# Kernel optimization log

Hardware: AMD Instinct MI355X
Metric: run time of the kernel (lower is better)

## Reference

```python
import jax, jax.numpy as jnp
import numpy as np

N = 100000      # nodes
E = 1600000     # edges (before self-loops)
D_IN = 128      # node_attr_size
H = 4           # gat_heads
C = 32          # hidden_size (per-head out channels)
F = H * C       # feature_size = 128
K = 16          # num_clusters
L = 2           # num_gat_layers
EPS = 1e-5
NEG_SLOPE = 0.2  # PyG GATv2Conv default leaky_relu slope


def setup_inputs() -> dict:
    key = jax.random.key(0)
    ks = jax.random.split(key, 8)
    x = jax.random.normal(ks[0], (N, D_IN), jnp.float32)
    edge_index = jax.random.randint(ks[1], (2, E), 0, N, jnp.int32)
    sF = 1.0 / np.sqrt(F).astype(np.float32)
    Wp = jax.random.normal(ks[2], (D_IN, F), jnp.float32) * (1.0 / np.sqrt(D_IN).astype(np.float32))
    bp = jnp.zeros((F,), jnp.float32)
    ln_g = jnp.ones((L, F), jnp.float32)
    ln_b = jnp.zeros((L, F), jnp.float32)
    Wl = jax.random.normal(ks[3], (L, F, H * C), jnp.float32) * sF
    bl = jnp.zeros((L, H * C), jnp.float32)
    Wr = jax.random.normal(ks[4], (L, F, H * C), jnp.float32) * sF
    br = jnp.zeros((L, H * C), jnp.float32)
    att = jax.random.normal(ks[5], (L, H, C), jnp.float32) * (1.0 / np.sqrt(C).astype(np.float32))
    gb = jnp.zeros((L, F), jnp.float32)  # GATv2Conv output bias
    Wc = jax.random.normal(ks[6], (F, K), jnp.float32) * sF
    bc = jnp.zeros((K,), jnp.float32)
    return dict(x=x, edge_index=edge_index, Wp=Wp, bp=bp, ln_g=ln_g, ln_b=ln_b,
                Wl=Wl, bl=bl, Wr=Wr, br=br, att=att, gb=gb, Wc=Wc, bc=bc)


def _layernorm(x, g, b):
    mu = jnp.mean(x, axis=-1, keepdims=True)
    var = jnp.var(x, axis=-1, keepdims=True)
    return (x - mu) * jax.lax.rsqrt(var + EPS) * g + b


def reference(x, edge_index, Wp, bp, ln_g, ln_b, Wl, bl, Wr, br, att, gb, Wc, bc):
    # GATv2Conv adds self-loops by default
    loops = jnp.arange(N, dtype=edge_index.dtype)
    src = jnp.concatenate([edge_index[0], loops])  # message source j
    dst = jnp.concatenate([edge_index[1], loops])  # message target i

    h = x @ Wp + bp  # node_feat_proj -> [N, F]
    for i in range(L):
        identity = h
        hn = _layernorm(h, ln_g[i], ln_b[i])
        x_l = (hn @ Wl[i] + bl[i]).reshape(N, H, C)  # source transform
        x_r = (hn @ Wr[i] + br[i]).reshape(N, H, C)  # target transform
        m = x_l[src] + x_r[dst]                       # [E+N, H, C]
        s = jnp.where(m > 0, m, NEG_SLOPE * m)        # leaky_relu(0.2)
        logits = jnp.einsum('ehc,hc->eh', s, att[i])  # [E+N, H]
        # segment softmax over incoming edges of each target node
        mx = jax.ops.segment_max(logits, dst, num_segments=N)
        a = jnp.exp(logits - mx[dst])
        den = jax.ops.segment_sum(a, dst, num_segments=N)
        alpha = a / den[dst]
        out = jax.ops.segment_sum(x_l[src] * alpha[:, :, None], dst, num_segments=N)
        out = out.reshape(N, F) + gb[i]
        # relu activation, dropout identity (eval), residual add
        h = jax.nn.relu(out) + identity

    classification_output = h @ Wc + bc
    return (classification_output, h)
```

## Files before the change

### kernel.cpp

```cpp
#include <hip/hip_runtime.h>
#include <hip/hip_bf16.h>
#include <math.h>
#include <stdint.h>

#define N_NODES 100000
#define N_EDGES 1600000
#define ET (N_EDGES + N_NODES)
#define FDIM 128
#define NK 16
#define EPS 1e-5f
#define SLOPE 0.2f

typedef __attribute__((ext_vector_type(8))) short bf16x8;
typedef __attribute__((ext_vector_type(4))) float f32x4;
typedef __attribute__((ext_vector_type(2))) _Float16 h2;

__device__ inline unsigned pk_bf16(float a, float b) {
    float2 f; f.x = a; f.y = b;
    __hip_bfloat162 t = __float22bfloat162_rn(f);
    return *reinterpret_cast<unsigned*>(&t);
}
__device__ inline h2 as_h2(unsigned u) { return __builtin_bit_cast(h2, u); }
__device__ inline unsigned as_u(h2 v) { return __builtin_bit_cast(unsigned, v); }

#define SWZ(X, P) __int_as_float(__builtin_amdgcn_ds_swizzle(__float_as_int(X), (P)))
#define DPPF(X, CTRL) __int_as_float(__builtin_amdgcn_mov_dpp(__float_as_int(X), (CTRL), 0xF, 0xF, true))
#define DX1(X) DPPF(X, 0xB1)
#define DX2(X) DPPF(X, 0x4E)
#define DR4(X) DPPF(X, 0x124)
#define DR8(X) DPPF(X, 0x128)
#define DB0(X) DPPF(X, 0x00)
#define DB1(X) DPPF(X, 0x55)
#define DB2(X) DPPF(X, 0xAA)
#define DB3(X) DPPF(X, 0xFF)

__device__ inline float exp2_hw(float x) {
    float r;
    asm("v_exp_f32 %0, %1" : "=v"(r) : "v"(x));
    return r;
}

#define FMAMIX_LO(ACC, U, W) \
    asm("v_fma_mix_f32 %0, %1, %2, %0 op_sel_hi:[1,0,0]" : "+v"(ACC) : "v"(U), "v"(W))
#define FMAMIX_HI(ACC, U, W) \
    asm("v_fma_mix_f32 %0, %1, %2, %0 op_sel:[1,0,0] op_sel_hi:[1,0,0]" : "+v"(ACC) : "v"(U), "v"(W))

__device__ inline int rflm(int v) { return __builtin_amdgcn_readfirstlane(v) & 131071; }


#define NBKT 196
#define BSH 9
#define BSTRIDE 10240
#define P1_EPT 8
#define P1_EPB (256 * P1_EPT)

__global__ __launch_bounds__(256) void part_kernel(const int* __restrict__ ei,
                                                   int* __restrict__ gcount,
                                                   int* __restrict__ staging) {
    __shared__ int hist[NBKT];
    __shared__ int lofs[NBKT];
    __shared__ int gbase[NBKT];
    __shared__ int s[256];
    __shared__ int spk[P1_EPB];
    __shared__ short sbk[P1_EPB];
    int t = threadIdx.x;
    if (t < NBKT) hist[t] = 0;
    __syncthreads();
    int e0 = blockIdx.x * P1_EPB + t;
    int pk[P1_EPT], bk[P1_EPT], rk[P1_EPT];
#pragma unroll
    for (int k = 0; k < P1_EPT; k++) {
        int e = e0 + k * 256;
        bk[k] = -1;
        if (e < ET) {
            int src, dst;
            if (e < N_EDGES) { src = ei[e]; dst = ei[N_EDGES + e]; }
            else             { src = dst = e - N_EDGES; }
            int b = dst >> BSH;
            pk[k] = (src << BSH) | (dst & 511);
            bk[k] = b;
            rk[k] = atomicAdd(&hist[b], 1);
        }
    }
    __syncthreads();
    int v = (t < NBKT) ? hist[t] : 0;
    s[t] = v;
    __syncthreads();
    for (int o = 1; o < 256; o <<= 1) {
        int add = (t >= o) ? s[t - o] : 0;
        __syncthreads();
        s[t] += add;
        __syncthreads();
    }
    if (t < NBKT) {
        lofs[t] = s[t] - v;
        gbase[t] = (v > 0) ? atomicAdd(&gcount[t], v) : 0;
    }
    __syncthreads();
#pragma unroll
    for (int k = 0; k < P1_EPT; k++) {
        if (bk[k] >= 0) {
            int idx = lofs[bk[k]] + rk[k];
            spk[idx] = pk[k];
            sbk[idx] = (short)bk[k];
        }
    }
    __syncthreads();
    int tot = lofs[NBKT - 1] + hist[NBKT - 1];
    for (int i = t; i < tot; i += 256) {
        int b = sbk[i];
        staging[b * BSTRIDE + gbase[b] + (i - lofs[b])] = spk[i];
    }
}

__global__ __launch_bounds__(1024) void bucket_csr_kernel(
        const int* __restrict__ staging, const int* __restrict__ gcount,
        int* __restrict__ off, int* __restrict__ perm) {
    __shared__ int hist[512];
    __shared__ int scn[512];
    __shared__ int cur[512];
    __shared__ int gpre[256];
    int b = blockIdx.x;
    int t = threadIdx.x;
    if (t < 512) hist[t] = 0;
    if (t < 256) gpre[t] = (t < NBKT) ? gcount[t] : 0;
    __syncthreads();
    int sz = gcount[b];
    for (int k = t; k < sz; k += 1024)
        atomicAdd(&hist[staging[b * BSTRIDE + k] & 511], 1);
    __syncthreads();
    int v = (t < 512) ? hist[t] : 0;
    if (t < 512) scn[t] = v;
    __syncthreads();
    for (int o = 1; o < 512; o <<= 1) {
        int add = 0, gadd = 0;
        int tg = t - 512;
        if (t < 512 && t >= o) add = scn[t - o];
        if (tg >= o && tg < 256 && o < 256) gadd = gpre[tg - o];
        __syncthreads();
        if (t < 512) scn[t] += add;
        if (tg >= o && tg < 256 && o < 256) gpre[tg] += gadd;
        __syncthreads();
    }
    int base = gpre[b] - sz;
    if (t < 512) {
        int excl = scn[t] - v;
        int n = (b << BSH) + t;
        if (n < N_NODES) off[n] = base + excl;
        cur[t] = excl;
    }
    if (b == 0 && t == 0) off[N_NODES] = ET;
    __syncthreads();
    for (int k = t; k < sz; k += 1024) {
        int p = staging[b * BSTRIDE + k];
        int slot = atomicAdd(&cur[p & 511], 1);
        perm[base + slot] = p >> BSH;
    }
}


__global__ void swizzle_kernel(const float* __restrict__ Wp,
                               const float* __restrict__ Wl,
                               const float* __restrict__ Wr,
                               ushort* __restrict__ wbp,
                               ushort* __restrict__ wbl0,
                               ushort* __restrict__ wbl1) {
    int bb = blockIdx.x, t = threadIdx.x;
    const float *W0, *W1; ushort* out; int nt;
    if (bb < 8)       { W0 = Wp; W1 = Wp; out = wbp; nt = bb; }
    else if (bb < 24) { W0 = Wl; W1 = Wr; out = wbl0; nt = bb - 8; }
    else              { W0 = Wl + FDIM * FDIM; W1 = Wr + FDIM * FDIM; out = wbl1; nt = bb - 24; }
    int kk = t >> 6, lane = t & 63;
    int n = nt * 16 + (lane & 15);
    int k0 = kk * 32 + (lane >> 4) * 8;
    const float* W = (n < 128) ? (W0 + n) : (W1 + (n - 128));
    float f[8];
#pragma unroll
    for (int j = 0; j < 8; j++) f[j] = W[(size_t)(k0 + j) * FDIM];
    uint4 u;
    u.x = pk_bf16(f[0], f[1]); u.y = pk_bf16(f[2], f[3]);
    u.z = pk_bf16(f[4], f[5]); u.w = pk_bf16(f[6], f[7]);
    *(uint4*)&out[(size_t)((nt * 4 + kk) * 64 + lane) * 8] = u;
}


__global__ __launch_bounds__(256) void ln_gemm2_kernel(
        const float* __restrict__ h,
        const float* __restrict__ g, const float* __restrict__ b,
        const ushort* __restrict__ wb, const float* __restrict__ bl,
        const float* __restrict__ br,
        ushort* __restrict__ xlh, ushort* __restrict__ xrh) {
    __shared__ uint4 fragbuf[4 * 272];
    int wid = (blockIdx.x * 256 + threadIdx.x) >> 6;
    int lane = threadIdx.x & 63;
    if (wid >= N_NODES / 16) return;
    uint4* fb = fragbuf + (threadIdx.x >> 6) * 272;
    int q = lane >> 4, m = lane & 15;
    int row0 = wid * 16;
    const float* hrow = h + (size_t)(row0 + m) * FDIM + q * 32;
    float v[32];
#pragma unroll
    for (int i = 0; i < 8; i++) {
        float4 t4 = *(const float4*)&hrow[i * 4];
        v[i * 4 + 0] = t4.x; v[i * 4 + 1] = t4.y; v[i * 4 + 2] = t4.z; v[i * 4 + 3] = t4.w;
    }
    float s = 0.f, ss = 0.f;
#pragma unroll
    for (int i = 0; i < 32; i++) { s += v[i]; ss += v[i] * v[i]; }
    s  += __shfl_xor(s, 16);  s  += __shfl_xor(s, 32);
    ss += __shfl_xor(ss, 16); ss += __shfl_xor(ss, 32);
    float mu = s * (1.f / 128.f);
    float var = ss * (1.f / 128.f) - mu * mu;
    float rv = rsqrtf(var + EPS);
#pragma unroll
    for (int i = 0; i < 8; i++) {
        float4 gv = *(const float4*)&g[q * 32 + i * 4];
        float4 bv = *(const float4*)&b[q * 32 + i * 4];
        v[i * 4 + 0] = (v[i * 4 + 0] - mu) * rv * gv.x + bv.x;
        v[i * 4 + 1] = (v[i * 4 + 1] - mu) * rv * gv.y + bv.y;
        v[i * 4 + 2] = (v[i * 4 + 2] - mu) * rv * gv.z + bv.z;
        v[i * 4 + 3] = (v[i * 4 + 3] - mu) * rv * gv.w + bv.w;
    }
#pragma unroll
    for (int p = 0; p < 4; p++) {
        uint4 u;
        u.x = pk_bf16(v[p * 8 + 0], v[p * 8 + 1]);
        u.y = pk_bf16(v[p * 8 + 2], v[p * 8 + 3]);
        u.z = pk_bf16(v[p * 8 + 4], v[p * 8 + 5]);
        u.w = pk_bf16(v[p * 8 + 6], v[p * 8 + 7]);
        fb[q * 68 + p * 17 + m] = u;
    }
    bf16x8 A[4];
#pragma unroll
    for (int kk = 0; kk < 4; kk++)
        A[kk] = *(const bf16x8*)&fb[kk * 68 + q * 17 + m];
    const bf16x8* wbv = (const bf16x8*)wb;
    f32x4 acc[16];
    f32x4 z = {0.f, 0.f, 0.f, 0.f};
#pragma unroll
    for (int nt = 0; nt < 16; nt++) acc[nt] = z;
#pragma unroll
    for (int nt = 0; nt < 16; nt++) {
#pragma unroll
        for (int kk = 0; kk < 4; kk++) {
            bf16x8 B = wbv[(nt * 4 + kk) * 64 + lane];
            acc[nt] = __builtin_amdgcn_mfma_f32_16x16x32_bf16(A[kk], B, acc[nt], 0, 0, 0);
        }
    }
#pragma unroll
    for (int nt = 0; nt < 16; nt++) {
        int col = nt * 16 + m;
        if (nt < 8) {
            float bias = bl[col];
#pragma unroll
            for (int r = 0; r < 4; r++) {
                _Float16 hf = (_Float16)(acc[nt][r] + bias);
                xlh[(size_t)(row0 + q * 4 + r) * FDIM + col] = __builtin_bit_cast(ushort, hf);
            }
        } else {
            int c2 = col - 128;
            float bias = br[c2];
#pragma unroll
            for (int r = 0; r < 4; r++) {
                _Float16 hf = (_Float16)(acc[nt][r] + bias);
                xrh[(size_t)(row0 + q * 4 + r) * FDIM + c2] = __builtin_bit_cast(ushort, hf);
            }
        }
    }
}

__global__ __launch_bounds__(256) void proj_kernel(
        const float* __restrict__ x, const ushort* __restrict__ wb,
        const float* __restrict__ bp, float* __restrict__ h) {
    __shared__ uint4 fragbuf[4 * 272];
    int wid = (blockIdx.x * 256 + threadIdx.x) >> 6;
    int lane = threadIdx.x & 63;
    if (wid >= N_NODES / 16) return;
    uint4* fb = fragbuf + (threadIdx.x >> 6) * 272;
    int q = lane >> 4, m = lane & 15;
    int row0 = wid * 16;
    const float* xrow = x + (size_t)(row0 + m) * FDIM + q * 32;
#pragma unroll
    for (int p = 0; p < 4; p++) {
        float4 a = *(const float4*)&xrow[p * 8];
        float4 c = *(const float4*)&xrow[p * 8 + 4];
        uint4 u;
        u.x = pk_bf16(a.x, a.y); u.y = pk_bf16(a.z, a.w);
        u.z = pk_bf16(c.x, c.y); u.w = pk_bf16(c.z, c.w);
        fb[q * 68 + p * 17 + m] = u;
    }
    bf16x8 A[4];
#pragma unroll
    for (int kk = 0; kk < 4; kk++)
        A[kk] = *(const bf16x8*)&fb[kk * 68 + q * 17 + m];
    const bf16x8* wbv = (const bf16x8*)wb;
    f32x4 acc[8];
    f32x4 z = {0.f, 0.f, 0.f, 0.f};
#pragma unroll
    for (int nt = 0; nt < 8; nt++) acc[nt] = z;
#pragma unroll
    for (int nt = 0; nt < 8; nt++) {
#pragma unroll
        for (int kk = 0; kk < 4; kk++) {
            bf16x8 B = wbv[(nt * 4 + kk) * 64 + lane];
            acc[nt] = __builtin_amdgcn_mfma_f32_16x16x32_bf16(A[kk], B, acc[nt], 0, 0, 0);
        }
    }
#pragma unroll
    for (int nt = 0; nt < 8; nt++) {
        int col = nt * 16 + m;
        float bias = bp[col];
#pragma unroll
        for (int r = 0; r < 4; r++)
            h[(size_t)(row0 + q * 4 + r) * FDIM + col] = acc[nt][r] + bias;
    }
}

__global__ __launch_bounds__(256) void final_kernel(const float* __restrict__ h,
                                                    const float* __restrict__ Wc,
                                                    const float* __restrict__ bc,
                                                    float* __restrict__ out) {
    __shared__ float sh[16][128];
    int row0 = blockIdx.x * 16;
    int t = threadIdx.x;
    for (int i = t; i < 512; i += 256) {
        int r = i >> 5, c4 = (i & 31) * 4;
        *(float4*)&sh[r][c4] = *(const float4*)&h[(size_t)(row0 + r) * FDIM + c4];
    }
    __syncthreads();
    int m = t >> 4, k = t & 15;
    float acc = 0.f;
    for (int c = 0; c < 128; c += 4) {
        const float4 xv = *(const float4*)&sh[m][c];
        acc += xv.x * Wc[(c + 0) * NK + k] + xv.y * Wc[(c + 1) * NK + k]
             + xv.z * Wc[(c + 2) * NK + k] + xv.w * Wc[(c + 3) * NK + k];
    }
    out[(size_t)(row0 + m) * NK + k] = acc + bc[k];
}


__global__ __launch_bounds__(256) void gat_agg_kernel(
        const unsigned* __restrict__ xlp, const unsigned* __restrict__ xrp,
        const int* __restrict__ off, const int* __restrict__ perm,
        const float* __restrict__ att, const float* __restrict__ gb,
        float* __restrict__ h) {
    int wave = (blockIdx.x * 256 + threadIdx.x) >> 6;
    unsigned lane = threadIdx.x & 63;
    if (wave >= N_NODES) return;
    int i = wave;
    h2 xrv = as_h2(xrp[(unsigned)i * 64u + lane]);
    const float2 hid = *(const float2*)&h[(size_t)i * FDIM + lane * 2];
    const float2 gbv = *(const float2*)&gb[lane * 2];
    float2 attf = *(const float2*)&att[lane * 2];
    h2 attp; attp[0] = (_Float16)(attf.x * 1.44269504f);
    attp[1] = (_Float16)(attf.y * 1.44269504f);
    const h2 c06 = {(_Float16)0.6f, (_Float16)0.6f};
    const h2 c04 = {(_Float16)0.4f, (_Float16)0.4f};
    bool b0 = lane & 1, b1 = lane & 2;
    int beg = __builtin_amdgcn_readfirstlane(off[i]);
    int end = __builtin_amdgcn_readfirstlane(off[i + 1]);
    float accx = 0.f, accy = 0.f, dloc = 0.f;
    const char* xlB = (const char*)xlp;
    unsigned laneB = lane << 2;

#define GLD(J) (*(const unsigned*)(xlB + ((unsigned)(J) * 256u + laneB)))

#define EDGE_PARTIAL(U, T)                                          \
    {                                                               \
        h2 mm = as_h2(U) + xrv;                                     \
        h2 am = as_h2(as_u(mm) & 0x7FFF7FFFu);                      \
        h2 sv = am * c04 + mm * c06;                                \
        T = __builtin_amdgcn_fdot2(sv, attp, 0.f, false);           \
    }

#define COMPUTE4(U0, U1, U2, U3)                                    \
    {                                                               \
        float t0, t1, t2, t3;                                       \
        EDGE_PARTIAL(U0, t0);                                       \
        EDGE_PARTIAL(U1, t1);                                       \
        EDGE_PARTIAL(U2, t2);                                       \
        EDGE_PARTIAL(U3, t3);                                       \
        float u   = b0 ? t1 : t0;                                   \
        float uu2 = b0 ? t0 : t1;                                   \
        u += DX1(uu2);                                              \
        float vv  = b0 ? t3 : t2;                                   \
        float vv2 = b0 ? t2 : t3;                                   \
        vv += DX1(vv2);                                             \
        float ww  = b1 ? vv : u;                                    \
        float ww2 = b1 ? u : vv;                                    \
        ww += DX2(ww2);                                             \
        ww += DR4(ww);                                              \
        ww += DR8(ww);                                              \
        float ew = exp2_hw(ww);                                     \
        dloc += ew;                                                 \
        float w0 = DB0(ew);                                         \
        float w1 = DB1(ew);                                         \
        float w2 = DB2(ew);                                         \
        float w3 = DB3(ew);                                         \
        FMAMIX_LO(accx, U0, w0); FMAMIX_HI(accy, U0, w0);           \
        FMAMIX_LO(accx, U1, w1); FMAMIX_HI(accy, U1, w1);           \
        FMAMIX_LO(accx, U2, w2); FMAMIX_HI(accy, U2, w2);           \
        FMAMIX_LO(accx, U3, w3); FMAMIX_HI(accy, U3, w3);           \
    }

#define TAIL1(U)                                                    \
    {                                                               \
        float tt;                                                   \
        EDGE_PARTIAL(U, tt);                                        \
        tt += DX1(tt);                                              \
        tt += DX2(tt);                                              \
        tt += DR4(tt);                                              \
        tt += DR8(tt);                                              \
        float w = exp2_hw(tt);                                      \
        if ((lane & 3) == 0) dloc += w;                             \
        FMAMIX_LO(accx, U, w); FMAMIX_HI(accy, U, w);               \
    }

    int nb = (end - beg) >> 2;
    int tl = (end - beg) & 3;
    unsigned c0, c1, c2, c3, d0, d1, d2, d3;
    unsigned t0v = 0, t1v = 0, t2v = 0;
    int4 p2;
    if (nb > 0) {
        int4 p0, p1;
        __builtin_memcpy(&p0, perm + beg, 16);
        __builtin_memcpy(&p1, perm + beg + 4, 16);
        __builtin_memcpy(&p2, perm + beg + 8, 16);
        c0 = GLD(rflm(p0.x)); c1 = GLD(rflm(p0.y)); c2 = GLD(rflm(p0.z)); c3 = GLD(rflm(p0.w));
        d0 = GLD(rflm(p1.x)); d1 = GLD(rflm(p1.y)); d2 = GLD(rflm(p1.z)); d3 = GLD(rflm(p1.w));
    }
    if (tl > 0) {
        int4 pt;
        __builtin_memcpy(&pt, perm + beg + 4 * nb, 16);
        t0v = GLD(rflm(pt.x));
        if (tl > 1) t1v = GLD(rflm(pt.y));
        if (tl > 2) t2v = GLD(rflm(pt.z));
    }
#pragma unroll 2
    for (int blk = 0; blk + 2 < nb; ++blk) {
        unsigned e0 = GLD(rflm(p2.x)), e1 = GLD(rflm(p2.y));
        unsigned e2 = GLD(rflm(p2.z)), e3 = GLD(rflm(p2.w));
        __builtin_memcpy(&p2, perm + beg + 4 * blk + 12, 16);
        COMPUTE4(c0, c1, c2, c3);
        c0 = d0; c1 = d1; c2 = d2; c3 = d3;
        d0 = e0; d1 = e1; d2 = e2; d3 = e3;
    }
    if (nb >= 2) {
        COMPUTE4(c0, c1, c2, c3);
        c0 = d0; c1 = d1; c2 = d2; c3 = d3;
    }
    if (nb >= 1) COMPUTE4(c0, c1, c2, c3);
    if (tl > 0) {
        TAIL1(t0v);
        if (tl > 1) TAIL1(t1v);
        if (tl > 2) TAIL1(t2v);
    }
#undef EDGE_PARTIAL
#undef COMPUTE4
#undef TAIL1
#undef GLD

    float den = dloc + DX1(dloc);
    den += DX2(den);
    float inv = 1.f / den;
    float ox = accx * inv + gbv.x;
    float oy = accy * inv + gbv.y;
    float2 res;
    res.x = fmaxf(ox, 0.f) + hid.x;
    res.y = fmaxf(oy, 0.f) + hid.y;
    *(float2*)&h[(size_t)i * FDIM + lane * 2] = res;
}


extern "C" void kernel_launch(void* const* d_in, const int* in_sizes, int n_in,
                              void* d_out, int out_size, void* d_ws, size_t ws_size,
                              hipStream_t stream) {
    const float* x    = (const float*)d_in[0];
    const int*   ei   = (const int*)  d_in[1];
    const float* Wp   = (const float*)d_in[2];
    const float* bp   = (const float*)d_in[3];
    const float* ln_g = (const float*)d_in[4];
    const float* ln_b = (const float*)d_in[5];
    const float* Wl   = (const float*)d_in[6];
    const float* bl   = (const float*)d_in[7];
    const float* Wr   = (const float*)d_in[8];
    const float* br   = (const float*)d_in[9];
    const float* att  = (const float*)d_in[10];
    const float* gb   = (const float*)d_in[11];
    const float* Wc   = (const float*)d_in[12];
    const float* bc   = (const float*)d_in[13];

    float* out_cls = (float*)d_out;
    float* h = out_cls + (size_t)N_NODES * NK;

    char* w = (char*)d_ws;
    int* off    = (int*)w; w += (size_t)(N_NODES + 1) * sizeof(int);
    int* gcount = (int*)w; w += 256 * sizeof(int);
    int* perm   = (int*)w; w += (size_t)ET * sizeof(int);
    uintptr_t a = ((uintptr_t)w + 255) & ~(uintptr_t)255;
    ushort* xlh = (ushort*)a;
    ushort* xrh = xlh + (size_t)N_NODES * FDIM;
    ushort* wbp = xrh + (size_t)N_NODES * FDIM;
    ushort* wbl0 = wbp + 8 * 4 * 64 * 8;
    ushort* wbl1 = wbl0 + 16 * 4 * 64 * 8;
    int* staging = (int*)xlh;

    swizzle_kernel<<<40, 256, 0, stream>>>(Wp, Wl, Wr, wbp, wbl0, wbl1);

    hipMemsetAsync(gcount, 0, NBKT * sizeof(int), stream);
    part_kernel<<<(ET + P1_EPB - 1) / P1_EPB, 256, 0, stream>>>(ei, gcount, staging);
    bucket_csr_kernel<<<NBKT, 1024, 0, stream>>>(staging, gcount, off, perm);

    const int gw = (N_NODES / 16 + 3) / 4;
    proj_kernel<<<gw, 256, 0, stream>>>(x, wbp, bp, h);

    for (int l = 0; l < 2; ++l) {
        ln_gemm2_kernel<<<gw, 256, 0, stream>>>(
            h, ln_g + l * FDIM, ln_b + l * FDIM,
            (l == 0) ? wbl0 : wbl1, bl + l * FDIM, br + l * FDIM,
            xlh, xrh);
        gat_agg_kernel<<<N_NODES / 4, 256, 0, stream>>>(
            (const unsigned*)xlh, (const unsigned*)xrh, off, perm,
            att + l * FDIM, gb + l * FDIM, h);
    }

    final_kernel<<<N_NODES / 16, 256, 0, stream>>>(h, Wc, bc, out_cls);
}
```

Before: 449.2 us.

## Process two destination nodes per wave in GAT aggregation with interleaved edge loops

The aggregation kernel now assigns two consecutive target nodes to each wavefront. It interleaves their edge gathers and softmax-weighted accumulations in a joint loop, then drains each node's remaining edges separately. The aim is more independent memory loads in flight per wave to hide gather latency, and halving the launched waves. The cost is higher register pressure and possible lower occupancy, plus serialized remainder loops when the two nodes' degrees differ.

```diff
diff --git a/kernel.cpp b/kernel.cpp
--- a/kernel.cpp
+++ b/kernel.cpp
@@ -23,7 +23,6 @@
 __device__ inline h2 as_h2(unsigned u) { return __builtin_bit_cast(h2, u); }
 __device__ inline unsigned as_u(h2 v) { return __builtin_bit_cast(unsigned, v); }
 
-#define SWZ(X, P) __int_as_float(__builtin_amdgcn_ds_swizzle(__float_as_int(X), (P)))
 #define DPPF(X, CTRL) __int_as_float(__builtin_amdgcn_mov_dpp(__float_as_int(X), (CTRL), 0xF, 0xF, true))
 #define DX1(X) DPPF(X, 0xB1)
 #define DX2(X) DPPF(X, 0x4E)
@@ -346,10 +345,15 @@
         float* __restrict__ h) {
     int wave = (blockIdx.x * 256 + threadIdx.x) >> 6;
     unsigned lane = threadIdx.x & 63;
-    if (wave >= N_NODES) return;
-    int i = wave;
-    h2 xrv = as_h2(xrp[(unsigned)i * 64u + lane]);
-    const float2 hid = *(const float2*)&h[(size_t)i * FDIM + lane * 2];
+    int iA = wave * 2;
+    if (iA >= N_NODES) return;
+    int iB = iA + 1;
+    int2 oA = *(const int2*)&off[iA];
+    int eB2 = off[iB + 1];
+    h2 xrvA = as_h2(xrp[(unsigned)iA * 64u + lane]);
+    h2 xrvB = as_h2(xrp[(unsigned)iB * 64u + lane]);
+    const float2 hidA = *(const float2*)&h[(size_t)iA * FDIM + lane * 2];
+    const float2 hidB = *(const float2*)&h[(size_t)iB * FDIM + lane * 2];
     const float2 gbv = *(const float2*)&gb[lane * 2];
     float2 attf = *(const float2*)&att[lane * 2];
     h2 attp; attp[0] = (_Float16)(attf.x * 1.44269504f);
@@ -357,29 +361,30 @@
     const h2 c06 = {(_Float16)0.6f, (_Float16)0.6f};
     const h2 c04 = {(_Float16)0.4f, (_Float16)0.4f};
     bool b0 = lane & 1, b1 = lane & 2;
-    int beg = __builtin_amdgcn_readfirstlane(off[i]);
-    int end = __builtin_amdgcn_readfirstlane(off[i + 1]);
-    float accx = 0.f, accy = 0.f, dloc = 0.f;
-    const char* xlB = (const char*)xlp;
+    int begA = __builtin_amdgcn_readfirstlane(oA.x);
+    int endA = __builtin_amdgcn_readfirstlane(oA.y);
+    int begB = endA;
+    int endB = __builtin_amdgcn_readfirstlane(eB2);
+    const char* xlB_ = (const char*)xlp;
     unsigned laneB = lane << 2;
 
-#define GLD(J) (*(const unsigned*)(xlB + ((unsigned)(J) * 256u + laneB)))
-
-#define EDGE_PARTIAL(U, T)                                          \
+#define GLD(J) (*(const unsigned*)(xlB_ + ((unsigned)(J) * 256u + laneB)))
+
+#define EDGE_PARTIAL(XRV, U, T)                                     \
     {                                                               \
-        h2 mm = as_h2(U) + xrv;                                     \
+        h2 mm = as_h2(U) + XRV;                                     \
         h2 am = as_h2(as_u(mm) & 0x7FFF7FFFu);                      \
         h2 sv = am * c04 + mm * c06;                                \
         T = __builtin_amdgcn_fdot2(sv, attp, 0.f, false);           \
     }
 
-#define COMPUTE4(U0, U1, U2, U3)                                    \
+#define COMPUTE4(S, U0, U1, U2, U3)                                 \
     {                                                               \
         float t0, t1, t2, t3;                                       \
-        EDGE_PARTIAL(U0, t0);                                       \
-        EDGE_PARTIAL(U1, t1);                                       \
-        EDGE_PARTIAL(U2, t2);                                       \
-        EDGE_PARTIAL(U3, t3);                                       \
+        EDGE_PARTIAL(xrv##S, U0, t0);                               \
+        EDGE_PARTIAL(xrv##S, U1, t1);                               \
+        EDGE_PARTIAL(xrv##S, U2, t2);                               \
+        EDGE_PARTIAL(xrv##S, U3, t3);                               \
         float u   = b0 ? t1 : t0;                                   \
         float uu2 = b0 ? t0 : t1;                                   \
         u += DX1(uu2);                                              \
@@ -392,83 +397,141 @@
         ww += DR4(ww);                                              \
         ww += DR8(ww);                                              \
         float ew = exp2_hw(ww);                                     \
-        dloc += ew;                                                 \
+        dloc##S += ew;                                              \
         float w0 = DB0(ew);                                         \
         float w1 = DB1(ew);                                         \
         float w2 = DB2(ew);                                         \
         float w3 = DB3(ew);                                         \
-        FMAMIX_LO(accx, U0, w0); FMAMIX_HI(accy, U0, w0);           \
-        FMAMIX_LO(accx, U1, w1); FMAMIX_HI(accy, U1, w1);           \
-        FMAMIX_LO(accx, U2, w2); FMAMIX_HI(accy, U2, w2);           \
-        FMAMIX_LO(accx, U3, w3); FMAMIX_HI(accy, U3, w3);           \
-    }
-
-#define TAIL1(U)                                                    \
+        FMAMIX_LO(accx##S, U0, w0); FMAMIX_HI(accy##S, U0, w0);     \
+        FMAMIX_LO(accx##S, U1, w1); FMAMIX_HI(accy##S, U1, w1);     \
+        FMAMIX_LO(accx##S, U2, w2); FMAMIX_HI(accy##S, U2, w2);     \
+        FMAMIX_LO(accx##S, U3, w3); FMAMIX_HI(accy##S, U3, w3);     \
+    }
+
+#define TAIL1(S, U)                                                 \
     {                                                               \
         float tt;                                                   \
-        EDGE_PARTIAL(U, tt);                                        \
+        EDGE_PARTIAL(xrv##S, U, tt);                                \
         tt += DX1(tt);                                              \
         tt += DX2(tt);                                              \
         tt += DR4(tt);                                              \
         tt += DR8(tt);                                              \
         float w = exp2_hw(tt);                                      \
-        if ((lane & 3) == 0) dloc += w;                             \
-        FMAMIX_LO(accx, U, w); FMAMIX_HI(accy, U, w);               \
-    }
-
-    int nb = (end - beg) >> 2;
-    int tl = (end - beg) & 3;
-    unsigned c0, c1, c2, c3, d0, d1, d2, d3;
-    unsigned t0v = 0, t1v = 0, t2v = 0;
-    int4 p2;
-    if (nb > 0) {
-        int4 p0, p1;
-        __builtin_memcpy(&p0, perm + beg, 16);
-        __builtin_memcpy(&p1, perm + beg + 4, 16);
-        __builtin_memcpy(&p2, perm + beg + 8, 16);
-        c0 = GLD(rflm(p0.x)); c1 = GLD(rflm(p0.y)); c2 = GLD(rflm(p0.z)); c3 = GLD(rflm(p0.w));
-        d0 = GLD(rflm(p1.x)); d1 = GLD(rflm(p1.y)); d2 = GLD(rflm(p1.z)); d3 = GLD(rflm(p1.w));
-    }
-    if (tl > 0) {
-        int4 pt;
-        __builtin_memcpy(&pt, perm + beg + 4 * nb, 16);
-        t0v = GLD(rflm(pt.x));
-        if (tl > 1) t1v = GLD(rflm(pt.y));
-        if (tl > 2) t2v = GLD(rflm(pt.z));
-    }
-#pragma unroll 2
-    for (int blk = 0; blk + 2 < nb; ++blk) {
-        unsigned e0 = GLD(rflm(p2.x)), e1 = GLD(rflm(p2.y));
-        unsigned e2 = GLD(rflm(p2.z)), e3 = GLD(rflm(p2.w));
-        __builtin_memcpy(&p2, perm + beg + 4 * blk + 12, 16);
-        COMPUTE4(c0, c1, c2, c3);
-        c0 = d0; c1 = d1; c2 = d2; c3 = d3;
-        d0 = e0; d1 = e1; d2 = e2; d3 = e3;
-    }
-    if (nb >= 2) {
-        COMPUTE4(c0, c1, c2, c3);
-        c0 = d0; c1 = d1; c2 = d2; c3 = d3;
-    }
-    if (nb >= 1) COMPUTE4(c0, c1, c2, c3);
-    if (tl > 0) {
-        TAIL1(t0v);
-        if (tl > 1) TAIL1(t1v);
-        if (tl > 2) TAIL1(t2v);
+        if ((lane & 3) == 0) dloc##S += w;                          \
+        FMAMIX_LO(accx##S, U, w); FMAMIX_HI(accy##S, U, w);         \
+    }
+
+    int nbA = (endA - begA) >> 2, tlA = (endA - begA) & 3;
+    int nbB = (endB - begB) >> 2, tlB = (endB - begB) & 3;
+    float accxA = 0.f, accyA = 0.f, dlocA = 0.f;
+    float accxB = 0.f, accyB = 0.f, dlocB = 0.f;
+    unsigned c0A, c1A, c2A, c3A, d0A, d1A, d2A, d3A; int4 p2A;
+    unsigned c0B, c1B, c2B, c3B, d0B, d1B, d2B, d3B; int4 p2B;
+    unsigned t0A = 0, t1A = 0, t2A = 0, t0B = 0, t1B = 0, t2B = 0;
+    int4 p0A, p1A, ptA, p0B, p1B, ptB;
+
+    if (nbA > 0) {
+        __builtin_memcpy(&p0A, perm + begA, 16);
+        __builtin_memcpy(&p1A, perm + begA + 4, 16);
+        __builtin_memcpy(&p2A, perm + begA + 8, 16);
+    }
+    if (tlA > 0) __builtin_memcpy(&ptA, perm + begA + 4 * nbA, 16);
+    if (nbB > 0) {
+        __builtin_memcpy(&p0B, perm + begB, 16);
+        __builtin_memcpy(&p1B, perm + begB + 4, 16);
+        __builtin_memcpy(&p2B, perm + begB + 8, 16);
+    }
+    if (tlB > 0) __builtin_memcpy(&ptB, perm + begB + 4 * nbB, 16);
+    if (nbA > 0) {
+        c0A = GLD(rflm(p0A.x)); c1A = GLD(rflm(p0A.y)); c2A = GLD(rflm(p0A.z)); c3A = GLD(rflm(p0A.w));
+        d0A = GLD(rflm(p1A.x)); d1A = GLD(rflm(p1A.y)); d2A = GLD(rflm(p1A.z)); d3A = GLD(rflm(p1A.w));
+    }
+    if (nbB > 0) {
+        c0B = GLD(rflm(p0B.x)); c1B = GLD(rflm(p0B.y)); c2B = GLD(rflm(p0B.z)); c3B = GLD(rflm(p0B.w));
+        d0B = GLD(rflm(p1B.x)); d1B = GLD(rflm(p1B.y)); d2B = GLD(rflm(p1B.z)); d3B = GLD(rflm(p1B.w));
+    }
+    if (tlA > 0) {
+        t0A = GLD(rflm(ptA.x));
+        if (tlA > 1) t1A = GLD(rflm(ptA.y));
+        if (tlA > 2) t2A = GLD(rflm(ptA.z));
+    }
+    if (tlB > 0) {
+        t0B = GLD(rflm(ptB.x));
+        if (tlB > 1) t1B = GLD(rflm(ptB.y));
+        if (tlB > 2) t2B = GLD(rflm(ptB.z));
+    }
+
+    int blkA = 0, blkB = 0;
+    while (blkA + 2 < nbA && blkB + 2 < nbB) {
+        unsigned e0 = GLD(rflm(p2A.x)), e1 = GLD(rflm(p2A.y));
+        unsigned e2 = GLD(rflm(p2A.z)), e3 = GLD(rflm(p2A.w));
+        unsigned f0 = GLD(rflm(p2B.x)), f1 = GLD(rflm(p2B.y));
+        unsigned f2 = GLD(rflm(p2B.z)), f3 = GLD(rflm(p2B.w));
+        __builtin_memcpy(&p2A, perm + begA + 4 * blkA + 12, 16);
+        __builtin_memcpy(&p2B, perm + begB + 4 * blkB + 12, 16);
+        COMPUTE4(A, c0A, c1A, c2A, c3A);
+        c0A = d0A; c1A = d1A; c2A = d2A; c3A = d3A;
+        d0A = e0; d1A = e1; d2A = e2; d3A = e3;
+        COMPUTE4(B, c0B, c1B, c2B, c3B);
+        c0B = d0B; c1B = d1B; c2B = d2B; c3B = d3B;
+        d0B = f0; d1B = f1; d2B = f2; d3B = f3;
+        ++blkA; ++blkB;
+    }
+    for (; blkA + 2 < nbA; ++blkA) {
+        unsigned e0 = GLD(rflm(p2A.x)), e1 = GLD(rflm(p2A.y));
+        unsigned e2 = GLD(rflm(p2A.z)), e3 = GLD(rflm(p2A.w));
+        __builtin_memcpy(&p2A, perm + begA + 4 * blkA + 12, 16);
+        COMPUTE4(A, c0A, c1A, c2A, c3A);
+        c0A = d0A; c1A = d1A; c2A = d2A; c3A = d3A;
+        d0A = e0; d1A = e1; d2A = e2; d3A = e3;
+    }
+    for (; blkB + 2 < nbB; ++blkB) {
+        unsigned f0 = GLD(rflm(p2B.x)), f1 = GLD(rflm(p2B.y));
+        unsigned f2 = GLD(rflm(p2B.z)), f3 = GLD(rflm(p2B.w));
+        __builtin_memcpy(&p2B, perm + begB + 4 * blkB + 12, 16);
+        COMPUTE4(B, c0B, c1B, c2B, c3B);
+        c0B = d0B; c1B = d1B; c2B = d2B; c3B = d3B;
+        d0B = f0; d1B = f1; d2B = f2; d3B = f3;
+    }
+    if (nbA >= 2) {
+        COMPUTE4(A, c0A, c1A, c2A, c3A);
+        c0A = d0A; c1A = d1A; c2A = d2A; c3A = d3A;
+    }
+    if (nbB >= 2) {
+        COMPUTE4(B, c0B, c1B, c2B, c3B);
+        c0B = d0B; c1B = d1B; c2B = d2B; c3B = d3B;
+    }
+    if (nbA >= 1) COMPUTE4(A, c0A, c1A, c2A, c3A);
+    if (nbB >= 1) COMPUTE4(B, c0B, c1B, c2B, c3B);
+    if (tlA > 0) {
+        TAIL1(A, t0A);
+        if (tlA > 1) TAIL1(A, t1A);
+        if (tlA > 2) TAIL1(A, t2A);
+    }
+    if (tlB > 0) {
+        TAIL1(B, t0B);
+        if (tlB > 1) TAIL1(B, t1B);
+        if (tlB > 2) TAIL1(B, t2B);
     }
 #undef EDGE_PARTIAL
 #undef COMPUTE4
 #undef TAIL1
 #undef GLD
 
-    float den = dloc + DX1(dloc);
-    den += DX2(den);
-    float inv = 1.f / den;
-    float ox = accx * inv + gbv.x;
-    float oy = accy * inv + gbv.y;
-    float2 res;
-    res.x = fmaxf(ox, 0.f) + hid.x;
-    res.y = fmaxf(oy, 0.f) + hid.y;
-    *(float2*)&h[(size_t)i * FDIM + lane * 2] = res;
+    float denA = dlocA + DX1(dlocA);
+    denA += DX2(denA);
+    float invA = 1.f / denA;
+    float2 resA;
+    resA.x = fmaxf(accxA * invA + gbv.x, 0.f) + hidA.x;
+    resA.y = fmaxf(accyA * invA + gbv.y, 0.f) + hidA.y;
+    *(float2*)&h[(size_t)iA * FDIM + lane * 2] = resA;
+    float denB = dlocB + DX1(dlocB);
+    denB += DX2(denB);
+    float invB = 1.f / denB;
+    float2 resB;
+    resB.x = fmaxf(accxB * invB + gbv.x, 0.f) + hidB.x;
+    resB.y = fmaxf(accyB * invB + gbv.y, 0.f) + hidB.y;
+    *(float2*)&h[(size_t)iB * FDIM + lane * 2] = resB;
 }
 
 
@@ -519,7 +582,7 @@
             h, ln_g + l * FDIM, ln_b + l * FDIM,
             (l == 0) ? wbl0 : wbl1, bl + l * FDIM, br + l * FDIM,
             xlh, xrh);
-        gat_agg_kernel<<<N_NODES / 4, 256, 0, stream>>>(
+        gat_agg_kernel<<<(N_NODES / 2) / 4, 256, 0, stream>>>(
             (const unsigned*)xlh, (const unsigned*)xrh, off, perm,
             att + l * FDIM, gb + l * FDIM, h);
     }
```

Result: no change. 451.8 us (+0.6%).
